# Performance work log

Measured on AMD Instinct MI355X. Metric: run time of the kernel, lower is better.

Reference implementation:

```python
import jax, jax.numpy as jnp
import numpy as np

B, P, ENC = 32, 197, 768
EMB, HID, ATT = 512, 512, 256
VOCAB, SLEN = 32000, 41


def setup_inputs() -> dict:
    key = jax.random.key(0)
    ks = jax.random.split(key, 24)
    s = lambda *sh: 1.0 / np.sqrt(sh[0])
    inp = {
        'encoder_out': jax.random.normal(ks[0], (B, P, ENC), dtype=jnp.float32),
        'captions': jax.random.randint(ks[1], (B, SLEN), 0, VOCAB),
        'emb': jax.random.normal(ks[2], (VOCAB, EMB), dtype=jnp.float32) * 0.02,
        # attention
        'W_ea': jax.random.normal(ks[3], (ENC, ATT), dtype=jnp.float32) * s(ENC),
        'b_ea': jnp.zeros((ATT,), jnp.float32),
        'W_da': jax.random.normal(ks[4], (HID, ATT), dtype=jnp.float32) * s(HID),
        'b_da': jnp.zeros((ATT,), jnp.float32),
        'w_fa': jax.random.normal(ks[5], (ATT,), dtype=jnp.float32) * s(ATT),
        'b_fa': jnp.zeros((), jnp.float32),
        # init h/c from mean encoder
        'W_inh': jax.random.normal(ks[6], (ENC, HID), dtype=jnp.float32) * s(ENC),
        'b_inh': jnp.zeros((HID,), jnp.float32),
        'W_inc': jax.random.normal(ks[7], (ENC, HID), dtype=jnp.float32) * s(ENC),
        'b_inc': jnp.zeros((HID,), jnp.float32),
        # gate
        'W_fb': jax.random.normal(ks[8], (HID, ENC), dtype=jnp.float32) * s(HID),
        'b_fb': jnp.zeros((ENC,), jnp.float32),
        # LSTMCell (PyTorch gate order: i, f, g, o)
        'W_ih': jax.random.normal(ks[9], (EMB + ENC, 4 * HID), dtype=jnp.float32) * s(EMB + ENC),
        'b_ih': jnp.zeros((4 * HID,), jnp.float32),
        'W_hh': jax.random.normal(ks[10], (HID, 4 * HID), dtype=jnp.float32) * s(HID),
        'b_hh': jnp.zeros((4 * HID,), jnp.float32),
        # output projection
        'W_out': jax.random.normal(ks[11], (HID, VOCAB), dtype=jnp.float32) * s(HID),
        'b_out': jnp.zeros((VOCAB,), jnp.float32),
    }
    return inp


def reference(encoder_out, captions, emb, W_ea, b_ea, W_da, b_da, w_fa, b_fa,
              W_inh, b_inh, W_inc, b_inc, W_fb, b_fb,
              W_ih, b_ih, W_hh, b_hh, W_out, b_out):
    # dropout is identity (eval mode / p used only in training stochasticity)
    mean_enc = encoder_out.mean(axis=1)                     # (B, ENC)
    h0 = mean_enc @ W_inh + b_inh                           # (B, HID)
    c0 = mean_enc @ W_inc + b_inc
    att1 = encoder_out @ W_ea + b_ea                        # (B, P, ATT) step-invariant
    embs = emb[captions]                                    # (B, S, EMB)
    T = captions.shape[1] - 1
    xs = jnp.swapaxes(embs[:, :T, :], 0, 1)                 # (T, B, EMB)

    def step(carry, x_t):
        h, c = carry
        att2 = h @ W_da + b_da                              # (B, ATT)
        e = jax.nn.relu(att1 + att2[:, None, :]) @ w_fa + b_fa  # (B, P)
        alpha = jax.nn.softmax(e, axis=1)
        awe = jnp.einsum('bp,bpd->bd', alpha, encoder_out)  # (B, ENC)
        gate = jax.nn.sigmoid(h @ W_fb + b_fb)
        awe = gate * awe
        lstm_in = jnp.concatenate([x_t, awe], axis=1)       # (B, EMB+ENC)
        gates = lstm_in @ W_ih + b_ih + h @ W_hh + b_hh     # (B, 4*HID)
        i, f, g, o = jnp.split(gates, 4, axis=1)
        c_new = jax.nn.sigmoid(f) * c + jax.nn.sigmoid(i) * jnp.tanh(g)
        h_new = jax.nn.sigmoid(o) * jnp.tanh(c_new)
        preds = h_new @ W_out + b_out                       # (B, VOCAB)
        return (h_new, c_new), preds

    _, preds = jax.lax.scan(step, (h0, c0), xs)             # (T, B, VOCAB)
    return jnp.swapaxes(preds, 0, 1)                        # (B, T, VOCAB)
```

## Files before the change

kernel.cpp:

```cpp
#include <hip/hip_runtime.h>

#define Bz   32
#define Pz   197
#define ENCz 768
#define EMBz 512
#define HIDz 512
#define ATTz 256
#define VOCz 32000
#define Tz   40

#define NBLK 224

typedef unsigned short ushort_t;
typedef __attribute__((ext_vector_type(8))) short frag_ab;
typedef __attribute__((ext_vector_type(4))) float frag_cd;
typedef __attribute__((ext_vector_type(4))) ushort_t ushort4v;
typedef __attribute__((ext_vector_type(8))) ushort_t ushort8v;

#define MFMA16(a, b, c) __builtin_amdgcn_mfma_f32_16x16x32_bf16((a), (b), (c), 0, 0, 0)

__device__ __forceinline__ float b2f(ushort_t u) {
    return __uint_as_float(((unsigned)u) << 16);
}
__device__ __forceinline__ ushort_t f2bf(float f) {
    unsigned u = __float_as_uint(f);
    unsigned r = (u + 0x7fffu + ((u >> 16) & 1u)) >> 16;
    return (ushort_t)r;
}
__device__ __forceinline__ float sigf(float x) { return 1.f / (1.f + __expf(-x)); }
__device__ __forceinline__ float tanhfast(float x) { return 1.f - 2.f / (__expf(2.f * x) + 1.f); }

__device__ __forceinline__ void st_f32(float* p, float v) {
    __hip_atomic_store(p, v, __ATOMIC_RELAXED, __HIP_MEMORY_SCOPE_AGENT);
}
__device__ __forceinline__ float ld_f32(const float* p) {
    return __hip_atomic_load(p, __ATOMIC_RELAXED, __HIP_MEMORY_SCOPE_AGENT);
}
__device__ __forceinline__ void st_u32(unsigned* p, unsigned v) {
    __hip_atomic_store(p, v, __ATOMIC_RELAXED, __HIP_MEMORY_SCOPE_AGENT);
}
__device__ __forceinline__ unsigned ld_u32(const unsigned* p) {
    return __hip_atomic_load(p, __ATOMIC_RELAXED, __HIP_MEMORY_SCOPE_AGENT);
}
__device__ __forceinline__ frag_ab ldfrag(const ushort_t* p) {
    union { frag_ab f; unsigned long long q[2]; } u;
    u.q[0] = __hip_atomic_load((const unsigned long long*)p, __ATOMIC_RELAXED, __HIP_MEMORY_SCOPE_AGENT);
    u.q[1] = __hip_atomic_load((const unsigned long long*)(p + 4), __ATOMIC_RELAXED, __HIP_MEMORY_SCOPE_AGENT);
    return u.f;
}

__device__ __forceinline__ void gbar(unsigned* flags, unsigned ep, int g, int tid) {
    __syncthreads();
    if (tid == 0) {
        asm volatile("s_waitcnt vmcnt(0)" ::: "memory");
        __hip_atomic_store(&flags[g << 5], ep, __ATOMIC_RELAXED, __HIP_MEMORY_SCOPE_AGENT);
    }
    if (tid < NBLK) {
        while (__hip_atomic_load(&flags[tid << 5], __ATOMIC_RELAXED, __HIP_MEMORY_SCOPE_AGENT) < ep)
            __builtin_amdgcn_s_sleep(1);
    }
    __syncthreads();
}

__global__ void k_binit(unsigned* f) {
    for (int i = threadIdx.x; i < NBLK * 32; i += 256) f[i] = 0u;
}

__global__ __launch_bounds__(256) void k_conv(const float* __restrict__ in, ushort_t* __restrict__ out) {
    size_t base = ((size_t)blockIdx.x * 256 + threadIdx.x) * 8;
    const float4* src = (const float4*)(in + base);
    float4 a = src[0], b = src[1];
    ushort8v v;
    v[0] = f2bf(a.x); v[1] = f2bf(a.y); v[2] = f2bf(a.z); v[3] = f2bf(a.w);
    v[4] = f2bf(b.x); v[5] = f2bf(b.y); v[6] = f2bf(b.z); v[7] = f2bf(b.w);
    *(ushort8v*)(out + base) = v;
}

__global__ __launch_bounds__(256) void k_mean(const float* __restrict__ enc, float* __restrict__ meanE) {
    int e = blockIdx.x * 256 + threadIdx.x;
    int b = e / ENCz, d = e % ENCz;
    const float* p = enc + (size_t)b * Pz * ENCz + d;
    float s = 0.f;
    for (int i = 0; i < Pz; ++i) s += p[i * ENCz];
    meanE[e] = s * (1.f / (float)Pz);
}

__global__ __launch_bounds__(256) void k_h0c0(const float* __restrict__ meanE,
                                              const float* __restrict__ W_inh, const float* __restrict__ b_inh,
                                              const float* __restrict__ W_inc, const float* __restrict__ b_inc,
                                              float* __restrict__ c_cur, ushort_t* __restrict__ Abuf) {
    __shared__ float msh[ENCz];
    int bid = blockIdx.x, tid = threadIdx.x;
    int b = bid >> 2, seg = bid & 3;
    for (int i = tid; i < ENCz; i += 256) msh[i] = meanE[b * ENCz + i];
    __syncthreads();
    int col = (seg & 1) * 256 + tid;
    bool isc = (seg >> 1) != 0;
    const float* W = isc ? W_inc : W_inh;
    const float* bb = isc ? b_inc : b_inh;
    float a0 = 0.f, a1 = 0.f, a2 = 0.f, a3 = 0.f;
    for (int k = 0; k < ENCz; k += 4) {
        a0 += msh[k + 0] * W[(k + 0) * HIDz + col];
        a1 += msh[k + 1] * W[(k + 1) * HIDz + col];
        a2 += msh[k + 2] * W[(k + 2) * HIDz + col];
        a3 += msh[k + 3] * W[(k + 3) * HIDz + col];
    }
    float acc = a0 + a1 + a2 + a3 + bb[col];
    if (isc) c_cur[b * HIDz + col] = acc;
    else Abuf[b * 1280 + 768 + col] = f2bf(acc);
}

__global__ __launch_bounds__(128) void k_gather(const int* __restrict__ captions, const float* __restrict__ emb,
                                                ushort_t* __restrict__ Xemb) {
    int row = blockIdx.x;
    int t = row >> 5, b = row & 31;
    int cap = captions[b * 41 + t];
    float4 f = *(const float4*)(emb + (size_t)cap * EMBz + threadIdx.x * 4);
    ushort4v v; v[0] = f2bf(f.x); v[1] = f2bf(f.y); v[2] = f2bf(f.z); v[3] = f2bf(f.w);
    *(ushort4v*)(Xemb + (size_t)row * EMBz + threadIdx.x * 4) = v;
}

__global__ __launch_bounds__(256) void k_transpose(const float* __restrict__ in, int R, int C,
                                                   ushort_t* __restrict__ out, int ldo, int koff) {
    __shared__ ushort_t tile[32][33];
    int c0 = blockIdx.x * 32, r0 = blockIdx.y * 32;
    int tx = threadIdx.x & 31, ty = threadIdx.x >> 5;
#pragma unroll
    for (int i = 0; i < 4; ++i) {
        int r = r0 + ty + i * 8;
        tile[ty + i * 8][tx] = f2bf(in[(size_t)r * C + c0 + tx]);
    }
    __syncthreads();
#pragma unroll
    for (int i = 0; i < 4; ++i) {
        int c = c0 + ty + i * 8;
        out[(size_t)c * ldo + koff + r0 + tx] = tile[tx][ty + i * 8];
    }
}

__global__ __launch_bounds__(256) void k_encTb(const float* __restrict__ enc, ushort_t* __restrict__ encTb) {
    __shared__ float tile[32][33];
    int b = blockIdx.z;
    int d0 = blockIdx.x * 32, p0 = blockIdx.y * 32;
    int tx = threadIdx.x & 31, ty = threadIdx.x >> 5;
#pragma unroll
    for (int i = 0; i < 4; ++i) {
        int p = p0 + ty + i * 8;
        tile[ty + i * 8][tx] = (p < Pz) ? enc[((size_t)b * Pz + p) * ENCz + d0 + tx] : 0.f;
    }
    __syncthreads();
#pragma unroll
    for (int i = 0; i < 4; ++i) {
        int d = d0 + ty + i * 8, p = p0 + tx;
        if (p < 200) encTb[((size_t)b * ENCz + d) * 200 + p] = f2bf(tile[tx][ty + i * 8]);
    }
}

template <int MODE>
__global__ __launch_bounds__(256) void k_gemm(const ushort_t* __restrict__ A, int lda, int M,
                                              const ushort_t* __restrict__ BT, int K,
                                              const float* __restrict__ B1, const float* __restrict__ B2,
                                              void* __restrict__ out, int ldo) {
    __shared__ __align__(16) ushort_t As[128 * 64];
    __shared__ __align__(16) ushort_t Bs[128 * 64];
    const int tid = threadIdx.x;
    const int lane = tid & 63, w = tid >> 6;
    const int wm = w >> 1, wn = w & 1;
    int n0, m0;
    if (MODE == 2) {
        const int total = gridDim.x * gridDim.y;
        const int lin = blockIdx.y * gridDim.x + blockIdx.x;
        const int q = total >> 3, r = total - (q << 3);
        const int xcd = lin & 7, slot = lin >> 3;
        const int L = (xcd < r) ? xcd * (q + 1) + slot : r * (q + 1) + (xcd - r) * q + slot;
        const int nIdx = L / (int)gridDim.y;
        n0 = nIdx * 128; m0 = (L - nIdx * (int)gridDim.y) * 128;
    } else {
        n0 = blockIdx.x * 128; m0 = blockIdx.y * 128;
    }
    const int quad = lane >> 4, c16 = lane & 15;

    frag_cd acc[4][4];
#pragma unroll
    for (int i = 0; i < 4; ++i)
#pragma unroll
        for (int j = 0; j < 4; ++j) acc[i][j] = (frag_cd){0.f, 0.f, 0.f, 0.f};

    for (int k0 = 0; k0 < K; k0 += 64) {
#pragma unroll
        for (int it = 0; it < 4; ++it) {
            int c = tid + it * 256;
            int row = c >> 3, col8 = (c & 7) * 8;
            int gr = m0 + row; gr = gr < M ? gr : M - 1;
            *(frag_ab*)&As[row * 64 + col8] = *(const frag_ab*)&A[(size_t)gr * lda + k0 + col8];
            *(frag_ab*)&Bs[row * 64 + col8] = *(const frag_ab*)&BT[(size_t)(n0 + row) * K + k0 + col8];
        }
        __syncthreads();
#pragma unroll
        for (int kk = 0; kk < 64; kk += 32) {
            int kcol = kk + quad * 8;
            frag_ab af[4], bf[4];
#pragma unroll
            for (int i = 0; i < 4; ++i) af[i] = *(const frag_ab*)&As[(wm * 64 + i * 16 + c16) * 64 + kcol];
#pragma unroll
            for (int j = 0; j < 4; ++j) bf[j] = *(const frag_ab*)&Bs[(wn * 64 + j * 16 + c16) * 64 + kcol];
#pragma unroll
            for (int i = 0; i < 4; ++i)
#pragma unroll
                for (int j = 0; j < 4; ++j) acc[i][j] = MFMA16(af[i], bf[j], acc[i][j]);
        }
        __syncthreads();
    }

#pragma unroll
    for (int i = 0; i < 4; ++i) {
#pragma unroll
        for (int j = 0; j < 4; ++j) {
            int n = n0 + wn * 64 + j * 16 + c16;
            float bias = B1[n];
            if (B2 != nullptr) bias += B2[n];
#pragma unroll
            for (int r = 0; r < 4; ++r) {
                int m = m0 + wm * 64 + i * 16 + quad * 4 + r;
                float v = acc[i][j][r] + bias;
                if (MODE == 0) {
                    if (m < M) ((float*)out)[(size_t)m * ldo + n] = v;
                } else if (MODE == 1) {
                    if (m < M) ((ushort_t*)out)[(size_t)m * ldo + n] = f2bf(v);
                } else {
                    int b = m & 31, t = m >> 5;
                    ((float*)out)[(size_t)b * (Tz * VOCz) + (size_t)t * VOCz + n] = v;
                }
            }
        }
    }
}

__device__ __forceinline__ void do_awe(int task, const ushort_t* encS, float* scratch,
                                       const float* gate_buf, const float* alpha_buf,
                                       ushort_t* Ab_r, int tid) {
    const int b = task >> 3, d0 = (task & 7) * 96;
    if (tid < 200) scratch[tid] = ld_f32(&alpha_buf[b * 200 + tid]);
    __syncthreads();
    if (tid < 192) {
        const int d = tid >> 1, h = tid & 1;
        const int c0 = h ? 13 : 0, c1 = h ? 25 : 13;
        float s = 0.f;
        for (int c = c0; c < c1; ++c) {
            ushort8v v = *(const ushort8v*)&encS[d * 200 + c * 8];
#pragma unroll
            for (int jj = 0; jj < 8; ++jj) s += b2f(v[jj]) * scratch[c * 8 + jj];
        }
        s += __shfl_xor(s, 1, 64);
        float gs = s * ld_f32(&gate_buf[b * 768 + d0 + d]);
        unsigned pk = f2bf(gs);
        unsigned nb = __shfl_down(pk, 2, 64);
        if ((tid & 3) == 0)
            st_u32((unsigned*)(Ab_r + b * 1280 + d0 + d), pk | (nb << 16));
    }
    __syncthreads();
}

__global__ __launch_bounds__(256, 1) void k_recur(
    const ushort_t* __restrict__ att1, const ushort_t* __restrict__ encTb,
    const ushort_t* __restrict__ W_preT, const float* __restrict__ b_da,
    const float* __restrict__ b_fb, const float* __restrict__ w_fa,
    const float* __restrict__ b_fa, const ushort_t* __restrict__ WgT,
    const float* __restrict__ Xih, const float* __restrict__ c0,
    ushort_t* __restrict__ Abuf, float* __restrict__ att2_buf,
    float* __restrict__ gate_buf, float* __restrict__ alpha_buf,
    ushort_t* __restrict__ Hall, unsigned* __restrict__ barflags)
{
    __shared__ __align__(16) char smem[126208];
    float* scratch = (float*)smem;
    char* R = smem + 8192;

    const int g = (int)blockIdx.x;
    const int tid = (int)threadIdx.x;
    const int lane = tid & 63, wv = tid >> 6;
    const int quad = lane >> 4, c16 = lane & 15;

    const bool isS3 = (g < 128);
    const bool isS1 = (g < 64);
    const bool isE  = (g >= 192);
    const int j0 = g << 2;

    ushort_t (*Wl)[1288] = (ushort_t(*)[1288])R;
    ushort_t* WpreL = (ushort_t*)(R + 41216);
    ushort_t* enc0  = isS1 ? (ushort_t*)(R + 57856)
                    : (isS3 ? (ushort_t*)(R + 41216) : (ushort_t*)R);
    ushort_t* enc1  = (ushort_t*)(R + 79616);
    ushort_t* att1L = (ushort_t*)R;

    if (isS3) {
        int r = tid >> 4, ch = tid & 15;
        int coln = ((r >> 2) << 9) + j0 + (r & 3);
        const ushort_t* src = WgT + (size_t)coln * 1280 + ch * 80;
        ushort_t* dst = &Wl[r][ch * 80];
#pragma unroll
        for (int i = 0; i < 10; ++i)
            *(ushort8v*)(dst + i * 8) = *(const ushort8v*)(src + i * 8);
    }
    if (isS1) {
        const int n0 = g << 4;
#pragma unroll
        for (int i = 0; i < 4; ++i) {
            int c = tid + i * 256;
            int r = c >> 6, col8 = (c & 63) * 8;
            *(ushort8v*)&WpreL[r * 520 + col8] = *(const ushort8v*)&W_preT[(size_t)(n0 + r) * 512 + col8];
        }
    }
    if (!isE) {
        const ushort_t* src = encTb + ((size_t)((g >> 3) * 768 + (g & 7) * 96)) * 200;
        for (int i = 0; i < 10; ++i) {
            int c = tid + i * 256;
            if (c < 2400) *(ushort8v*)&enc0[c * 8] = *(const ushort8v*)&src[c * 8];
        }
        if (g >= 64 && g < 128) {
            int task1 = 192 + (g - 64);
            const ushort_t* src1 = encTb + ((size_t)((task1 >> 3) * 768 + (task1 & 7) * 96)) * 200;
            for (int i = 0; i < 10; ++i) {
                int c = tid + i * 256;
                if (c < 2400) *(ushort8v*)&enc1[c * 8] = *(const ushort8v*)&src1[c * 8];
            }
        }
    } else {
        const int eb = g - 192;
        for (int i = 0; i < 25; ++i) {
            int c = tid + i * 256;
            if (c < 6304) {
                int p = c >> 5, off = (c & 31) * 8;
                *(ushort8v*)&att1L[p * 264 + off] = *(const ushort8v*)&att1[((size_t)(eb * Pz + p)) * 256 + off];
            }
        }
    }
    float creg = 0.f;
    if (isS3 && tid < 128) creg = c0[(tid >> 2) * HIDz + j0 + (tid & 3)];
    __syncthreads();

    unsigned bt = 0;
    for (int t = 0; t < Tz; ++t) {
        ushort_t* Ab_r = Abuf + (size_t)(t & 1) * 40960;
        ushort_t* Ab_w = Abuf + (size_t)((t + 1) & 1) * 40960;

        if (isS1) {
            const int n0 = g << 4;
            frag_cd a0 = (frag_cd){0.f, 0.f, 0.f, 0.f};
            frag_cd a1 = (frag_cd){0.f, 0.f, 0.f, 0.f};
            const ushort_t* Wp = WpreL + (size_t)c16 * 520;
            const ushort_t* Ah = Ab_r + 768;
            const int kbase = wv * 128 + quad * 8;
#pragma unroll
            for (int kk = 0; kk < 4; ++kk) {
                const int kcol = kbase + kk * 32;
                frag_ab bfr = *(const frag_ab*)&Wp[kcol];
                a0 = MFMA16(ldfrag(&Ah[c16 * 1280 + kcol]), bfr, a0);
                a1 = MFMA16(ldfrag(&Ah[(16 + c16) * 1280 + kcol]), bfr, a1);
            }
#pragma unroll
            for (int r = 0; r < 4; ++r) {
                scratch[wv * 512 + (quad * 4 + r) * 16 + c16] = a0[r];
                scratch[wv * 512 + 256 + (quad * 4 + r) * 16 + c16] = a1[r];
            }
            __syncthreads();
#pragma unroll
            for (int h = 0; h < 2; ++h) {
                int idx = tid + h * 256;
                int m = idx >> 4, nl = idx & 15, n = n0 + nl;
                int base = (m >> 4) * 256 + (m & 15) * 16 + nl;
                float v = scratch[base] + scratch[512 + base] +
                          scratch[1024 + base] + scratch[1536 + base];
                if (n < 256) st_f32(&att2_buf[m * 256 + n], v + b_da[n]);
                else st_f32(&gate_buf[m * 768 + n - 256], sigf(v + b_fb[n - 256]));
            }
        }
        gbar(barflags, ++bt, g, tid);

        if (isE) {
            const int eb = g - 192;
            scratch[tid] = ld_f32(&att2_buf[eb * 256 + tid]);
            scratch[256 + tid] = w_fa[tid];
            __syncthreads();
            float ev = -3.0e38f;
            if (tid < Pz) {
                const ushort_t* ar = att1L + tid * 264;
                float s = 0.f;
#pragma unroll
                for (int j8 = 0; j8 < 256; j8 += 8) {
                    ushort8v v = *(const ushort8v*)&ar[j8];
#pragma unroll
                    for (int jj = 0; jj < 8; ++jj)
                        s += fmaxf(b2f(v[jj]) + scratch[j8 + jj], 0.f) * scratch[256 + j8 + jj];
                }
                ev = s + b_fa[0];
            }
            float mv = ev;
            for (int o = 32; o; o >>= 1) mv = fmaxf(mv, __shfl_down(mv, o, 64));
            if (lane == 0) scratch[512 + wv] = mv;
            __syncthreads();
            const float mx = fmaxf(fmaxf(scratch[512], scratch[513]), fmaxf(scratch[514], scratch[515]));
            float ex = (tid < Pz) ? __expf(ev - mx) : 0.f;
            float sv = ex;
            for (int o = 32; o; o >>= 1) sv += __shfl_down(sv, o, 64);
            if (lane == 0) scratch[516 + wv] = sv;
            __syncthreads();
            const float inv = 1.f / (scratch[516] + scratch[517] + scratch[518] + scratch[519]);
            if (tid < 200) st_f32(&alpha_buf[eb * 200 + tid], ex * inv);
        }
        gbar(barflags, ++bt, g, tid);

        if (!isE) {
            do_awe(g, enc0, scratch, gate_buf, alpha_buf, Ab_r, tid);
            if (g >= 64 && g < 128)
                do_awe(192 + (g - 64), enc1, scratch, gate_buf, alpha_buf, Ab_r, tid);
        }
        gbar(barflags, ++bt, g, tid);

        if (isS3) {
            frag_cd p0 = (frag_cd){0.f, 0.f, 0.f, 0.f};
            frag_cd p1 = (frag_cd){0.f, 0.f, 0.f, 0.f};
            const ushort_t* Ar0 = Ab_r + (size_t)c16 * 1280 + wv * 320 + quad * 8;
            const ushort_t* Ar1 = Ar0 + 16 * 1280;
            const ushort_t* Wr = &Wl[c16][wv * 320 + quad * 8];
#pragma unroll
            for (int ks = 0; ks < 10; ++ks) {
                frag_ab bfr = *(const frag_ab*)(Wr + ks * 32);
                p0 = MFMA16(ldfrag(Ar0 + ks * 32), bfr, p0);
                p1 = MFMA16(ldfrag(Ar1 + ks * 32), bfr, p1);
            }
#pragma unroll
            for (int r = 0; r < 4; ++r) {
                scratch[wv * 512 + (quad * 4 + r) * 16 + c16] = p0[r];
                scratch[wv * 512 + 256 + (quad * 4 + r) * 16 + c16] = p1[r];
            }
            __syncthreads();
            float s0, s1;
            {
                const int mr = tid >> 4, col = tid & 15;
                const int base = mr * 16 + col;
                const int xcol = ((col >> 2) << 9) + j0 + (col & 3);
                s0 = scratch[base] + scratch[512 + base] + scratch[1024 + base] + scratch[1536 + base]
                   + Xih[(size_t)t * 65536 + mr * 2048 + xcol];
                s1 = scratch[256 + base] + scratch[768 + base] + scratch[1280 + base] + scratch[1792 + base]
                   + Xih[(size_t)t * 65536 + (16 + mr) * 2048 + xcol];
            }
            __syncthreads();
            scratch[tid] = s0;
            scratch[256 + tid] = s1;
            __syncthreads();
            if (tid < 128) {
                const int bl = tid >> 2, jj = tid & 3, j = j0 + jj;
                const float iv = scratch[bl * 16 + jj], fv = scratch[bl * 16 + 4 + jj];
                const float gv = scratch[bl * 16 + 8 + jj], ov = scratch[bl * 16 + 12 + jj];
                const float cn = sigf(fv) * creg + sigf(iv) * tanhfast(gv);
                creg = cn;
                const float hn = sigf(ov) * tanhfast(cn);
                const ushort_t hb = f2bf(hn);
                Hall[((size_t)t * 32 + bl) * HIDz + j] = hb;
                unsigned pk = hb;
                unsigned nb = __shfl_down(pk, 1, 64);
                if ((tid & 1) == 0)
                    st_u32((unsigned*)(Ab_w + bl * 1280 + 768 + j), pk | (nb << 16));
            }
        }
        if (t < Tz - 1) gbar(barflags, ++bt, g, tid);
    }
}

extern "C" void kernel_launch(void* const* d_in, const int* in_sizes, int n_in,
                              void* d_out, int out_size, void* d_ws, size_t ws_size,
                              hipStream_t stream) {
    const float* enc   = (const float*)d_in[0];
    const int*   caps  = (const int*)d_in[1];
    const float* emb   = (const float*)d_in[2];
    const float* W_ea  = (const float*)d_in[3];
    const float* b_ea  = (const float*)d_in[4];
    const float* W_da  = (const float*)d_in[5];
    const float* b_da  = (const float*)d_in[6];
    const float* w_fa  = (const float*)d_in[7];
    const float* b_fa  = (const float*)d_in[8];
    const float* W_inh = (const float*)d_in[9];
    const float* b_inh = (const float*)d_in[10];
    const float* W_inc = (const float*)d_in[11];
    const float* b_inc = (const float*)d_in[12];
    const float* W_fb  = (const float*)d_in[13];
    const float* b_fb  = (const float*)d_in[14];
    const float* W_ih  = (const float*)d_in[15];
    const float* b_ih  = (const float*)d_in[16];
    const float* W_hh  = (const float*)d_in[17];
    const float* b_hh  = (const float*)d_in[18];
    const float* W_out = (const float*)d_in[19];
    const float* b_out = (const float*)d_in[20];

    char* ws = (char*)d_ws;
    ushort_t* att1     = (ushort_t*)(ws + 0);
    ushort_t* Xemb     = (ushort_t*)(ws + 3227648);
    ushort_t* encB     = (ushort_t*)(ws + 4538368);
    float*    Xih      = (float*)(ws + 14221312);
    float*    meanE    = (float*)(ws + 24707072);
    float*    c_cur    = (float*)(ws + 24805376);
    ushort_t* Abuf     = (ushort_t*)(ws + 24870912);
    float*    att2_buf = (float*)(ws + 25034752);
    float*    gate_buf = (float*)(ws + 25067520);
    float*    alpha_buf= (float*)(ws + 25165824);
    ushort_t* Hall     = (ushort_t*)(ws + 25191424);
    ushort_t* WgT      = (ushort_t*)(ws + 26502144);
    ushort_t* W_preT   = (ushort_t*)(ws + 31745024);
    ushort_t* W_eaT    = (ushort_t*)(ws + 32793600);
    ushort_t* W_ihxT   = (ushort_t*)(ws + 33186816);
    ushort_t* W_outT   = (ushort_t*)(ws + 35283968);
    ushort_t* encTb    = (ushort_t*)(ws + 68051968);
    unsigned* barflags = (unsigned*)(ws + 77882368);

    k_binit<<<1, 256, 0, stream>>>(barflags);
    k_conv<<<2364, 256, 0, stream>>>(enc, encB);
    k_mean<<<96, 256, 0, stream>>>(enc, meanE);
    k_h0c0<<<128, 256, 0, stream>>>(meanE, W_inh, b_inh, W_inc, b_inc, c_cur, Abuf);
    k_gather<<<1280, 128, 0, stream>>>(caps, emb, Xemb);
    k_encTb<<<dim3(24, 7, 32), 256, 0, stream>>>(enc, encTb);
    k_transpose<<<dim3(8, 24), 256, 0, stream>>>(W_ea, 768, 256, W_eaT, 768, 0);
    k_transpose<<<dim3(64, 16), 256, 0, stream>>>(W_ih, 512, 2048, W_ihxT, 512, 0);
    k_transpose<<<dim3(64, 24), 256, 0, stream>>>(W_ih + 512 * 2048, 768, 2048, WgT, 1280, 0);
    k_transpose<<<dim3(64, 16), 256, 0, stream>>>(W_hh, 512, 2048, WgT, 1280, 768);
    k_transpose<<<dim3(8, 16), 256, 0, stream>>>(W_da, 512, 256, W_preT, 512, 0);
    k_transpose<<<dim3(24, 16), 256, 0, stream>>>(W_fb, 512, 768, W_preT + 256 * 512, 512, 0);
    k_transpose<<<dim3(1000, 16), 256, 0, stream>>>(W_out, 512, 32000, W_outT, 512, 0);

    k_gemm<1><<<dim3(2, 50), 256, 0, stream>>>(encB, 768, 6304, W_eaT, 768, b_ea, nullptr, att1, 256);
    k_gemm<0><<<dim3(16, 10), 256, 0, stream>>>(Xemb, 512, 1280, W_ihxT, 512, b_ih, b_hh, Xih, 2048);

    hipLaunchKernelGGL(k_recur, dim3(NBLK), dim3(256), 0, stream,
                       att1, encTb, W_preT, b_da, b_fb, w_fa, b_fa, WgT, Xih,
                       c_cur, Abuf, att2_buf, gate_buf, alpha_buf, Hall, barflags);

    k_gemm<2><<<dim3(250, 10), 256, 0, stream>>>(Hall, 512, 1280, W_outT, 512, b_out, nullptr, d_out, VOCz);
}
```

Before: 1.394 ms.

## Replace global barriers with point-to-point flags and recompute att2/gate locally

After: 1.462 ms. +4.8%, slower.

```diff
diff --git a/kernel.cpp b/kernel.cpp
--- a/kernel.cpp
+++ b/kernel.cpp
@@ -48,41 +48,54 @@
     u.q[1] = __hip_atomic_load((const unsigned long long*)(p + 4), __ATOMIC_RELAXED, __HIP_MEMORY_SCOPE_AGENT);
     return u.f;
 }
-
-__device__ __forceinline__ void gbar(unsigned* flags, unsigned ep, int g, int tid) {
+__device__ __forceinline__ void arrive(unsigned* slot, unsigned v, int tid) {
     __syncthreads();
     if (tid == 0) {
         asm volatile("s_waitcnt vmcnt(0)" ::: "memory");
-        __hip_atomic_store(&flags[g << 5], ep, __ATOMIC_RELAXED, __HIP_MEMORY_SCOPE_AGENT);
-    }
-    if (tid < NBLK) {
-        while (__hip_atomic_load(&flags[tid << 5], __ATOMIC_RELAXED, __HIP_MEMORY_SCOPE_AGENT) < ep)
-            __builtin_amdgcn_s_sleep(1);
-    }
-    __syncthreads();
+        st_u32(slot, v);
+    }
 }
 
 __global__ void k_binit(unsigned* f) {
-    for (int i = threadIdx.x; i < NBLK * 32; i += 256) f[i] = 0u;
-}
-
-__global__ __launch_bounds__(256) void k_conv(const float* __restrict__ in, ushort_t* __restrict__ out) {
-    size_t base = ((size_t)blockIdx.x * 256 + threadIdx.x) * 8;
-    const float4* src = (const float4*)(in + base);
-    float4 a = src[0], b = src[1];
-    ushort8v v;
-    v[0] = f2bf(a.x); v[1] = f2bf(a.y); v[2] = f2bf(a.z); v[3] = f2bf(a.w);
-    v[4] = f2bf(b.x); v[5] = f2bf(b.y); v[6] = f2bf(b.z); v[7] = f2bf(b.w);
-    *(ushort8v*)(out + base) = v;
-}
-
-__global__ __launch_bounds__(256) void k_mean(const float* __restrict__ enc, float* __restrict__ meanE) {
-    int e = blockIdx.x * 256 + threadIdx.x;
-    int b = e / ENCz, d = e % ENCz;
-    const float* p = enc + (size_t)b * Pz * ENCz + d;
-    float s = 0.f;
-    for (int i = 0; i < Pz; ++i) s += p[i * ENCz];
-    meanE[e] = s * (1.f / (float)Pz);
+    for (int i = threadIdx.x; i < 11264; i += 256) f[i] = 0u;
+}
+
+__global__ __launch_bounds__(256) void k_prep(const float* __restrict__ enc, ushort_t* __restrict__ encB,
+                                              float* __restrict__ meanE, ushort_t* __restrict__ encTb) {
+    __shared__ float tile[32][33];
+    const int bid = blockIdx.x, tid = threadIdx.x;
+    if (bid < 2364) {
+        size_t base = ((size_t)bid * 256 + tid) * 8;
+        const float4* src = (const float4*)(enc + base);
+        float4 a = src[0], b = src[1];
+        ushort8v v;
+        v[0] = f2bf(a.x); v[1] = f2bf(a.y); v[2] = f2bf(a.z); v[3] = f2bf(a.w);
+        v[4] = f2bf(b.x); v[5] = f2bf(b.y); v[6] = f2bf(b.z); v[7] = f2bf(b.w);
+        *(ushort8v*)(encB + base) = v;
+    } else if (bid < 2460) {
+        int e = (bid - 2364) * 256 + tid;
+        int b = e / ENCz, d = e % ENCz;
+        const float* p = enc + (size_t)b * Pz * ENCz + d;
+        float s = 0.f;
+        for (int i = 0; i < Pz; ++i) s += p[i * ENCz];
+        meanE[e] = s * (1.f / (float)Pz);
+    } else {
+        int idx = bid - 2460;
+        int d0 = (idx % 24) * 32; int rest = idx / 24;
+        int p0 = (rest % 7) * 32; int b = rest / 7;
+        int tx = tid & 31, ty = tid >> 5;
+#pragma unroll
+        for (int i = 0; i < 4; ++i) {
+            int p = p0 + ty + i * 8;
+            tile[ty + i * 8][tx] = (p < Pz) ? enc[((size_t)b * Pz + p) * ENCz + d0 + tx] : 0.f;
+        }
+        __syncthreads();
+#pragma unroll
+        for (int i = 0; i < 4; ++i) {
+            int d = d0 + ty + i * 8, p = p0 + tx;
+            if (p < 200) encTb[((size_t)b * ENCz + d) * 200 + p] = f2bf(tile[tx][ty + i * 8]);
+        }
+    }
 }
 
 __global__ __launch_bounds__(256) void k_h0c0(const float* __restrict__ meanE,
@@ -135,24 +148,6 @@
     for (int i = 0; i < 4; ++i) {
         int c = c0 + ty + i * 8;
         out[(size_t)c * ldo + koff + r0 + tx] = tile[tx][ty + i * 8];
-    }
-}
-
-__global__ __launch_bounds__(256) void k_encTb(const float* __restrict__ enc, ushort_t* __restrict__ encTb) {
-    __shared__ float tile[32][33];
-    int b = blockIdx.z;
-    int d0 = blockIdx.x * 32, p0 = blockIdx.y * 32;
-    int tx = threadIdx.x & 31, ty = threadIdx.x >> 5;
-#pragma unroll
-    for (int i = 0; i < 4; ++i) {
-        int p = p0 + ty + i * 8;
-        tile[ty + i * 8][tx] = (p < Pz) ? enc[((size_t)b * Pz + p) * ENCz + d0 + tx] : 0.f;
-    }
-    __syncthreads();
-#pragma unroll
-    for (int i = 0; i < 4; ++i) {
-        int d = d0 + ty + i * 8, p = p0 + tx;
-        if (p < 200) encTb[((size_t)b * ENCz + d) * 200 + p] = f2bf(tile[tx][ty + i * 8]);
     }
 }
 
@@ -236,12 +231,29 @@
     }
 }
 
-__device__ __forceinline__ void do_awe(int task, const ushort_t* encS, float* scratch,
-                                       const float* gate_buf, const float* alpha_buf,
-                                       ushort_t* Ab_r, int tid) {
-    const int b = task >> 3, d0 = (task & 7) * 96;
-    if (tid < 200) scratch[tid] = ld_f32(&alpha_buf[b * 200 + tid]);
-    __syncthreads();
+__device__ __forceinline__ void gate_calc(const ushort_t* __restrict__ W_preT, const float* __restrict__ b_fb,
+                                          const float* hsh, int d0, float* gate_out, int tid) {
+    if (tid < 192) {
+        const int d = tid >> 1, half = tid & 1;
+        const ushort_t* wr = W_preT + (size_t)(256 + d0 + d) * 512 + half * 256;
+        const float* hh = hsh + half * 256;
+        float a0 = 0.f, a1 = 0.f;
+        for (int k = 0; k < 256; k += 8) {
+            ushort8v wv8 = *(const ushort8v*)&wr[k];
+#pragma unroll
+            for (int x = 0; x < 8; ++x) {
+                float f = b2f(wv8[x]) * hh[k + x];
+                if (x & 1) a1 += f; else a0 += f;
+            }
+        }
+        float s = a0 + a1;
+        s += __shfl_xor(s, 1, 64);
+        if (half == 0) gate_out[d] = sigf(s + b_fb[d0 + d]);
+    }
+}
+
+__device__ __forceinline__ void awe_dot(const ushort_t* encS, const float* gate_l, const float* alpha_l,
+                                        ushort_t* dst, int tid) {
     if (tid < 192) {
         const int d = tid >> 1, h = tid & 1;
         const int c0 = h ? 13 : 0, c1 = h ? 25 : 13;
@@ -249,16 +261,14 @@
         for (int c = c0; c < c1; ++c) {
             ushort8v v = *(const ushort8v*)&encS[d * 200 + c * 8];
 #pragma unroll
-            for (int jj = 0; jj < 8; ++jj) s += b2f(v[jj]) * scratch[c * 8 + jj];
+            for (int jj = 0; jj < 8; ++jj) s += b2f(v[jj]) * alpha_l[c * 8 + jj];
         }
         s += __shfl_xor(s, 1, 64);
-        float gs = s * ld_f32(&gate_buf[b * 768 + d0 + d]);
+        float gs = s * gate_l[d];
         unsigned pk = f2bf(gs);
         unsigned nb = __shfl_down(pk, 2, 64);
-        if ((tid & 3) == 0)
-            st_u32((unsigned*)(Ab_r + b * 1280 + d0 + d), pk | (nb << 16));
-    }
-    __syncthreads();
+        if ((tid & 3) == 0) st_u32((unsigned*)(dst + d), pk | (nb << 16));
+    }
 }
 
 __global__ __launch_bounds__(256, 1) void k_recur(
@@ -267,29 +277,35 @@
     const float* __restrict__ b_fb, const float* __restrict__ w_fa,
     const float* __restrict__ b_fa, const ushort_t* __restrict__ WgT,
     const float* __restrict__ Xih, const float* __restrict__ c0,
-    ushort_t* __restrict__ Abuf, float* __restrict__ att2_buf,
-    float* __restrict__ gate_buf, float* __restrict__ alpha_buf,
+    ushort_t* __restrict__ Abuf, float* __restrict__ alpha_buf,
     ushort_t* __restrict__ Hall, unsigned* __restrict__ barflags)
 {
     __shared__ __align__(16) char smem[126208];
     float* scratch = (float*)smem;
     char* R = smem + 8192;
 
+    unsigned* flagS = barflags;
+    unsigned* flagA = barflags + 4096;
+    unsigned* flagE = barflags + 10240;
+
     const int g = (int)blockIdx.x;
     const int tid = (int)threadIdx.x;
     const int lane = tid & 63, wv = tid >> 6;
     const int quad = lane >> 4, c16 = lane & 15;
 
     const bool isS3 = (g < 128);
-    const bool isS1 = (g < 64);
     const bool isE  = (g >= 192);
+    const bool dual = (g >= 128 && g < 192);
     const int j0 = g << 2;
+    const int task0 = g;
+    const int task1 = dual ? 192 + (g - 128) : 0;
+    const int b0 = task0 >> 3, d0 = (task0 & 7) * 96;
+    const int b1 = task1 >> 3, d1 = (task1 & 7) * 96;
+    const int eb = g - 192;
 
     ushort_t (*Wl)[1288] = (ushort_t(*)[1288])R;
-    ushort_t* WpreL = (ushort_t*)(R + 41216);
-    ushort_t* enc0  = isS1 ? (ushort_t*)(R + 57856)
-                    : (isS3 ? (ushort_t*)(R + 41216) : (ushort_t*)R);
-    ushort_t* enc1  = (ushort_t*)(R + 79616);
+    ushort_t* enc0  = isS3 ? (ushort_t*)(R + 41216) : (ushort_t*)R;
+    ushort_t* enc1  = (ushort_t*)(R + 38400);
     ushort_t* att1L = (ushort_t*)R;
 
     if (isS3) {
@@ -301,31 +317,20 @@
         for (int i = 0; i < 10; ++i)
             *(ushort8v*)(dst + i * 8) = *(const ushort8v*)(src + i * 8);
     }
-    if (isS1) {
-        const int n0 = g << 4;
-#pragma unroll
-        for (int i = 0; i < 4; ++i) {
-            int c = tid + i * 256;
-            int r = c >> 6, col8 = (c & 63) * 8;
-            *(ushort8v*)&WpreL[r * 520 + col8] = *(const ushort8v*)&W_preT[(size_t)(n0 + r) * 512 + col8];
-        }
-    }
     if (!isE) {
-        const ushort_t* src = encTb + ((size_t)((g >> 3) * 768 + (g & 7) * 96)) * 200;
+        const ushort_t* src = encTb + ((size_t)(b0 * 768 + (task0 & 7) * 96)) * 200;
         for (int i = 0; i < 10; ++i) {
             int c = tid + i * 256;
             if (c < 2400) *(ushort8v*)&enc0[c * 8] = *(const ushort8v*)&src[c * 8];
         }
-        if (g >= 64 && g < 128) {
-            int task1 = 192 + (g - 64);
-            const ushort_t* src1 = encTb + ((size_t)((task1 >> 3) * 768 + (task1 & 7) * 96)) * 200;
+        if (dual) {
+            const ushort_t* src1 = encTb + ((size_t)(b1 * 768 + (task1 & 7) * 96)) * 200;
             for (int i = 0; i < 10; ++i) {
                 int c = tid + i * 256;
                 if (c < 2400) *(ushort8v*)&enc1[c * 8] = *(const ushort8v*)&src1[c * 8];
             }
         }
     } else {
-        const int eb = g - 192;
         for (int i = 0; i < 25; ++i) {
             int c = tid + i * 256;
             if (c < 6304) {
@@ -338,48 +343,38 @@
     if (isS3 && tid < 128) creg = c0[(tid >> 2) * HIDz + j0 + (tid & 3)];
     __syncthreads();
 
-    unsigned bt = 0;
     for (int t = 0; t < Tz; ++t) {
         ushort_t* Ab_r = Abuf + (size_t)(t & 1) * 40960;
         ushort_t* Ab_w = Abuf + (size_t)((t + 1) & 1) * 40960;
-
-        if (isS1) {
-            const int n0 = g << 4;
-            frag_cd a0 = (frag_cd){0.f, 0.f, 0.f, 0.f};
-            frag_cd a1 = (frag_cd){0.f, 0.f, 0.f, 0.f};
-            const ushort_t* Wp = WpreL + (size_t)c16 * 520;
-            const ushort_t* Ah = Ab_r + 768;
-            const int kbase = wv * 128 + quad * 8;
-#pragma unroll
-            for (int kk = 0; kk < 4; ++kk) {
-                const int kcol = kbase + kk * 32;
-                frag_ab bfr = *(const frag_ab*)&Wp[kcol];
-                a0 = MFMA16(ldfrag(&Ah[c16 * 1280 + kcol]), bfr, a0);
-                a1 = MFMA16(ldfrag(&Ah[(16 + c16) * 1280 + kcol]), bfr, a1);
-            }
-#pragma unroll
-            for (int r = 0; r < 4; ++r) {
-                scratch[wv * 512 + (quad * 4 + r) * 16 + c16] = a0[r];
-                scratch[wv * 512 + 256 + (quad * 4 + r) * 16 + c16] = a1[r];
-            }
-            __syncthreads();
-#pragma unroll
-            for (int h = 0; h < 2; ++h) {
-                int idx = tid + h * 256;
-                int m = idx >> 4, nl = idx & 15, n = n0 + nl;
-                int base = (m >> 4) * 256 + (m & 15) * 16 + nl;
-                float v = scratch[base] + scratch[512 + base] +
-                          scratch[1024 + base] + scratch[1536 + base];
-                if (n < 256) st_f32(&att2_buf[m * 256 + n], v + b_da[n]);
-                else st_f32(&gate_buf[m * 768 + n - 256], sigf(v + b_fb[n - 256]));
-            }
-        }
-        gbar(barflags, ++bt, g, tid);
+        const unsigned epoch = (unsigned)(t + 1);
 
         if (isE) {
-            const int eb = g - 192;
-            scratch[tid] = ld_f32(&att2_buf[eb * 256 + tid]);
-            scratch[256 + tid] = w_fa[tid];
+            if (t) {
+                if (tid < 128) while (ld_u32(&flagS[tid << 5]) < (unsigned)t) __builtin_amdgcn_s_sleep(1);
+                __syncthreads();
+            }
+            if (tid < 64) {
+                frag_ab v = ldfrag(Ab_r + eb * 1280 + 768 + tid * 8);
+#pragma unroll
+                for (int i = 0; i < 8; ++i) scratch[tid * 8 + i] = b2f((ushort_t)v[i]);
+            }
+            __syncthreads();
+            {
+                const ushort_t* wr = W_preT + (size_t)tid * 512;
+                float a0 = 0.f, a1 = 0.f, a2 = 0.f, a3 = 0.f;
+                for (int k = 0; k < 512; k += 16) {
+                    ushort8v w0 = *(const ushort8v*)&wr[k];
+                    ushort8v w1 = *(const ushort8v*)&wr[k + 8];
+#pragma unroll
+                    for (int x = 0; x < 8; ++x) {
+                        float f0 = b2f(w0[x]) * scratch[k + x];
+                        float f1 = b2f(w1[x]) * scratch[k + 8 + x];
+                        if (x & 1) { a1 += f0; a3 += f1; } else { a0 += f0; a2 += f1; }
+                    }
+                }
+                scratch[512 + tid] = (a0 + a1) + (a2 + a3) + b_da[tid];
+                scratch[768 + tid] = w_fa[tid];
+            }
             __syncthreads();
             float ev = -3.0e38f;
             if (tid < Pz) {
@@ -390,33 +385,61 @@
                     ushort8v v = *(const ushort8v*)&ar[j8];
 #pragma unroll
                     for (int jj = 0; jj < 8; ++jj)
-                        s += fmaxf(b2f(v[jj]) + scratch[j8 + jj], 0.f) * scratch[256 + j8 + jj];
+                        s += fmaxf(b2f(v[jj]) + scratch[512 + j8 + jj], 0.f) * scratch[768 + j8 + jj];
                 }
                 ev = s + b_fa[0];
             }
             float mv = ev;
             for (int o = 32; o; o >>= 1) mv = fmaxf(mv, __shfl_down(mv, o, 64));
-            if (lane == 0) scratch[512 + wv] = mv;
-            __syncthreads();
-            const float mx = fmaxf(fmaxf(scratch[512], scratch[513]), fmaxf(scratch[514], scratch[515]));
+            if (lane == 0) scratch[1024 + wv] = mv;
+            __syncthreads();
+            const float mx = fmaxf(fmaxf(scratch[1024], scratch[1025]), fmaxf(scratch[1026], scratch[1027]));
             float ex = (tid < Pz) ? __expf(ev - mx) : 0.f;
             float sv = ex;
             for (int o = 32; o; o >>= 1) sv += __shfl_down(sv, o, 64);
-            if (lane == 0) scratch[516 + wv] = sv;
-            __syncthreads();
-            const float inv = 1.f / (scratch[516] + scratch[517] + scratch[518] + scratch[519]);
+            if (lane == 0) scratch[1028 + wv] = sv;
+            __syncthreads();
+            const float inv = 1.f / (scratch[1028] + scratch[1029] + scratch[1030] + scratch[1031]);
             if (tid < 200) st_f32(&alpha_buf[eb * 200 + tid], ex * inv);
-        }
-        gbar(barflags, ++bt, g, tid);
-
-        if (!isE) {
-            do_awe(g, enc0, scratch, gate_buf, alpha_buf, Ab_r, tid);
-            if (g >= 64 && g < 128)
-                do_awe(192 + (g - 64), enc1, scratch, gate_buf, alpha_buf, Ab_r, tid);
-        }
-        gbar(barflags, ++bt, g, tid);
+            arrive(&flagE[eb << 5], epoch, tid);
+        } else {
+            if (t) {
+                if (tid < 128) while (ld_u32(&flagS[tid << 5]) < (unsigned)t) __builtin_amdgcn_s_sleep(1);
+                __syncthreads();
+            }
+            if (tid < 64) {
+                frag_ab v = ldfrag(Ab_r + b0 * 1280 + 768 + tid * 8);
+#pragma unroll
+                for (int i = 0; i < 8; ++i) scratch[tid * 8 + i] = b2f((ushort_t)v[i]);
+            }
+            if (dual && tid >= 64 && tid < 128) {
+                int tt = tid - 64;
+                frag_ab v = ldfrag(Ab_r + b1 * 1280 + 768 + tt * 8);
+#pragma unroll
+                for (int i = 0; i < 8; ++i) scratch[512 + tt * 8 + i] = b2f((ushort_t)v[i]);
+            }
+            __syncthreads();
+            gate_calc(W_preT, b_fb, scratch, d0, scratch + 1024, tid);
+            if (dual) gate_calc(W_preT, b_fb, scratch + 512, d1, scratch + 1120, tid);
+            __syncthreads();
+            if (tid == 0)  while (ld_u32(&flagE[b0 << 5]) < epoch) __builtin_amdgcn_s_sleep(1);
+            if (dual && tid == 32) while (ld_u32(&flagE[b1 << 5]) < epoch) __builtin_amdgcn_s_sleep(1);
+            __syncthreads();
+            if (tid < 200) scratch[1280 + tid] = ld_f32(&alpha_buf[b0 * 200 + tid]);
+            __syncthreads();
+            awe_dot(enc0, scratch + 1024, scratch + 1280, Ab_r + b0 * 1280 + d0, tid);
+            if (dual) {
+                __syncthreads();
+                if (tid < 200) scratch[1280 + tid] = ld_f32(&alpha_buf[b1 * 200 + tid]);
+                __syncthreads();
+                awe_dot(enc1, scratch + 1120, scratch + 1280, Ab_r + b1 * 1280 + d1, tid);
+            }
+            arrive(&flagA[g << 5], epoch, tid);
+        }
 
         if (isS3) {
+            if (tid < 192) while (ld_u32(&flagA[tid << 5]) < epoch) __builtin_amdgcn_s_sleep(1);
+            __syncthreads();
             frag_cd p0 = (frag_cd){0.f, 0.f, 0.f, 0.f};
             frag_cd p1 = (frag_cd){0.f, 0.f, 0.f, 0.f};
             const ushort_t* Ar0 = Ab_r + (size_t)c16 * 1280 + wv * 320 + quad * 8;
@@ -462,8 +485,8 @@
                 if ((tid & 1) == 0)
                     st_u32((unsigned*)(Ab_w + bl * 1280 + 768 + j), pk | (nb << 16));
             }
-        }
-        if (t < Tz - 1) gbar(barflags, ++bt, g, tid);
+            arrive(&flagS[g << 5], epoch, tid);
+        }
     }
 }
 
@@ -500,8 +523,6 @@
     float*    meanE    = (float*)(ws + 24707072);
     float*    c_cur    = (float*)(ws + 24805376);
     ushort_t* Abuf     = (ushort_t*)(ws + 24870912);
-    float*    att2_buf = (float*)(ws + 25034752);
-    float*    gate_buf = (float*)(ws + 25067520);
     float*    alpha_buf= (float*)(ws + 25165824);
     ushort_t* Hall     = (ushort_t*)(ws + 25191424);
     ushort_t* WgT      = (ushort_t*)(ws + 26502144);
@@ -513,11 +534,9 @@
     unsigned* barflags = (unsigned*)(ws + 77882368);
 
     k_binit<<<1, 256, 0, stream>>>(barflags);
-    k_conv<<<2364, 256, 0, stream>>>(enc, encB);
-    k_mean<<<96, 256, 0, stream>>>(enc, meanE);
+    k_prep<<<7836, 256, 0, stream>>>(enc, encB, meanE, encTb);
     k_h0c0<<<128, 256, 0, stream>>>(meanE, W_inh, b_inh, W_inc, b_inc, c_cur, Abuf);
     k_gather<<<1280, 128, 0, stream>>>(caps, emb, Xemb);
-    k_encTb<<<dim3(24, 7, 32), 256, 0, stream>>>(enc, encTb);
     k_transpose<<<dim3(8, 24), 256, 0, stream>>>(W_ea, 768, 256, W_eaT, 768, 0);
     k_transpose<<<dim3(64, 16), 256, 0, stream>>>(W_ih, 512, 2048, W_ihxT, 512, 0);
     k_transpose<<<dim3(64, 24), 256, 0, stream>>>(W_ih + 512 * 2048, 768, 2048, WgT, 1280, 0);
@@ -531,7 +550,7 @@
 
     hipLaunchKernelGGL(k_recur, dim3(NBLK), dim3(256), 0, stream,
                        att1, encTb, W_preT, b_da, b_fb, w_fa, b_fa, WgT, Xih,
-                       c_cur, Abuf, att2_buf, gate_buf, alpha_buf, Hall, barflags);
+                       c_cur, Abuf, alpha_buf, Hall, barflags);
 
     k_gemm<2><<<dim3(250, 10), 256, 0, stream>>>(Hall, 512, 1280, W_outT, 512, b_out, nullptr, d_out, VOCz);
 }
```
